# Performance work log

Hardware: AMD Instinct MI355X
Metric: run time of the kernel (lower is better)

The kernel has to match this reference:

```python
import jax, jax.numpy as jnp
import numpy as np

GROUP_MANTISSA = 8
GROUP_SIZE = 36


def bfp_quantize(x, mantissa=GROUP_MANTISSA, group_size=GROUP_SIZE):
    """Block floating point: flatten, group consecutive group_size elements,
    share the max exponent within each group, keep `mantissa` mantissa bits."""
    flat = x.reshape(-1)
    n = flat.shape[0]
    pad = (-n) % group_size
    f = jnp.pad(flat, (0, pad)).reshape(-1, group_size)  # [G, group_size]
    m = jnp.max(jnp.abs(f), axis=1, keepdims=True)       # group max magnitude
    safe_m = jnp.where(m > 0, m, jnp.ones_like(m))
    e = jnp.floor(jnp.log2(safe_m))                      # shared exponent
    scale = jnp.exp2(e - (mantissa - 1))                 # LSB step for the group
    q = jnp.round(f / scale) * scale
    q = jnp.where(m > 0, q, jnp.zeros_like(q))
    return q.reshape(-1)[:n].reshape(x.shape)


def setup_inputs() -> dict:
    key = jax.random.key(0)
    kx, kw, kb = jax.random.split(key, 3)
    x = jax.random.normal(kx, (32, 64, 112, 112), dtype=jnp.float32)
    # kaiming-uniform-ish scale for a 3x3x64 fan-in
    fan_in = 64 * 3 * 3
    bound = 1.0 / np.sqrt(fan_in)
    weight = jax.random.uniform(kw, (64, 64, 3, 3), dtype=jnp.float32, minval=-bound, maxval=bound) * np.sqrt(3.0)
    bias = jax.random.uniform(kb, (64,), dtype=jnp.float32, minval=-bound, maxval=bound)
    return {"x": x, "weight": weight, "bias": bias}


def reference(x, weight, bias):
    xq = bfp_quantize(x)
    wq = bfp_quantize(weight)
    out = jax.lax.conv_general_dilated(
        xq, wq,
        window_strides=(1, 1),
        padding=((1, 1), (1, 1)),
        lhs_dilation=(1, 1),
        rhs_dilation=(1, 1),
        dimension_numbers=("NCHW", "OIHW", "NCHW"),
        feature_group_count=1,
    )
    return out + bias[None, :, None, None]
```

## Files before the change

kernel.cpp:

```cpp
#include <hip/hip_runtime.h>
#include <hip/hip_bf16.h>

typedef __attribute__((ext_vector_type(4))) float f32x4;
typedef __attribute__((ext_vector_type(8))) short s16x8;

#define X_ELEMS 25690112
#define X_F4    6422528
#define NG_FULL 713614
#define NG      713615
#define HW 112
#define CHW (64*112*112)

__device__ __forceinline__ unsigned short f32_to_bf16_exact(float q) {
    return (unsigned short)(__float_as_uint(q) >> 16);
}

__device__ __forceinline__ void scale_from_max(float m, float& scale, float& inv) {
    if (m > 0.f) {
        int e = (int)((__float_as_uint(m) >> 23) & 0xFF) - 127;
        scale = __builtin_ldexpf(1.0f, e - 7);
        inv   = __builtin_ldexpf(1.0f, 7 - e);
    } else { scale = 0.f; inv = 0.f; }
}

__global__ __launch_bounds__(256) void q1_scales(const float* __restrict__ x,
                                                 float2* __restrict__ sc) {
    __shared__ float lmax[2304];
    int b = blockIdx.x, tid = threadIdx.x;
    long base4 = (long)b * 2304;
    #pragma unroll
    for (int it = 0; it < 9; ++it) {
        int i = it * 256 + tid;
        long g4 = base4 + i;
        float m = 0.f;
        if (g4 < X_F4) {
            float4 v = ((const float4*)x)[g4];
            m = fmaxf(fmaxf(fabsf(v.x), fabsf(v.y)), fmaxf(fabsf(v.z), fabsf(v.w)));
        }
        lmax[i] = m;
    }
    __syncthreads();
    int g = b * 256 + tid;
    if (g < NG) {
        float m = 0.f;
        int o = tid * 9;
        #pragma unroll
        for (int j = 0; j < 9; ++j) m = fmaxf(m, lmax[o + j]);
        float s, inv; scale_from_max(m, s, inv);
        sc[g] = make_float2(s, inv);
    }
}

__global__ __launch_bounds__(256) void qw_kernel(const float* __restrict__ w,
                                                 unsigned short* __restrict__ wt) {
    int g = blockIdx.x * 256 + threadIdx.x;
    if (g >= 1024) return;
    const float4* p = (const float4*)w + g * 9;
    float vv[36]; float m = 0.f;
    #pragma unroll
    for (int i = 0; i < 9; ++i) {
        float4 v = p[i];
        vv[i*4+0]=v.x; vv[i*4+1]=v.y; vv[i*4+2]=v.z; vv[i*4+3]=v.w;
        m = fmaxf(m, fmaxf(fmaxf(fabsf(v.x), fabsf(v.y)), fmaxf(fabsf(v.z), fabsf(v.w))));
    }
    float s, inv; scale_from_max(m, s, inv);
    #pragma unroll
    for (int j = 0; j < 36; ++j) {
        int flat = g * 36 + j;
        int k = flat / 576, rem = flat % 576;
        int c = rem / 9, pp = rem % 9;
        float q = rintf(vv[j] * inv) * s;
        wt[pp * 4096 + k * 64 + c] = f32_to_bf16_exact(q);
    }
}

__global__ __launch_bounds__(256) void q2_quant(const float* __restrict__ x,
                                               const float2* __restrict__ sc,
                                               unsigned short* __restrict__ xt) {
    int n = blockIdx.y, h = blockIdx.x;
    int tid = threadIdx.x;
    int cg = tid >> 7;
    int wv = tid & 127;
    if (wv >= HW) return;
    int base = n * CHW + h * HW + wv;
    int ob = ((n * HW + h) * HW + wv) * 64 + cg * 32;
    #pragma unroll
    for (int jo = 0; jo < 4; ++jo) {
        union { unsigned short u[8]; uint4 d; } pk;
        #pragma unroll
        for (int j = 0; j < 8; ++j) {
            int c = cg * 32 + jo * 8 + j;
            unsigned off = (unsigned)(base + c * 12544);
            float v = x[off];
            float2 s = sc[off / 36u];
            pk.u[j] = f32_to_bf16_exact(rintf(v * s.y) * s.x);
        }
        *(uint4*)(xt + ob + jo * 8) = pk.d;
    }
}

__global__ __launch_bounds__(256, 2) void conv_mfma(const unsigned short* __restrict__ xt,
                                                    const unsigned short* __restrict__ wt,
                                                    const float* __restrict__ bias,
                                                    float* __restrict__ out) {
    __shared__ unsigned short xs[300 * 72];
    const int tid = threadIdx.x;
    const int wave = tid >> 6, lane = tid & 63;
    const int wl = lane & 15, quad = lane >> 4;
    const int kg = wave & 1, mg = wave >> 1;
    const int b = blockIdx.x;
    const int n = b / 56, rem = b % 56;
    const int h0 = (rem >> 2) * 8, w0 = (rem & 3) * 28;

    #pragma unroll
    for (int it = 0; it < 10; ++it) {
        int q = it * 256 + tid;
        if (q < 2400) {
            int pixel = q >> 3, sub = q & 7;
            int r = pixel / 30, col = pixel % 30;
            int hh = h0 + r - 1, ww = w0 + col - 1;
            uint4 v = {0u, 0u, 0u, 0u};
            if (hh >= 0 && hh < HW && ww >= 0 && ww < HW)
                v = *(const uint4*)(xt + (((n * HW + hh) * HW + ww) << 6) + sub * 8);
            *(uint4*)&xs[pixel * 72 + sub * 8] = v;
        }
    }

    s16x8 Bf[9][2][2];
    #pragma unroll
    for (int p = 0; p < 9; ++p)
        #pragma unroll
        for (int cs = 0; cs < 2; ++cs)
            #pragma unroll
            for (int j = 0; j < 2; ++j)
                Bf[p][cs][j] = *(const s16x8*)(wt + p * 4096 +
                                ((kg * 2 + j) * 16 + wl) * 64 + cs * 32 + quad * 8);

    float bv[2];
    #pragma unroll
    for (int j = 0; j < 2; ++j) bv[j] = bias[kg * 32 + j * 16 + wl];

    int pixb[7], eofs[7];
    #pragma unroll
    for (int mti = 0; mti < 7; ++mti) {
        int m = (mg * 7 + mti) * 16 + wl;
        pixb[mti] = (m / 28) * 30 + (m % 28);
        int m0 = (mg * 7 + mti) * 16 + quad * 4;
        eofs[mti] = (m0 / 28) * HW + (m0 % 28);
    }

    __syncthreads();

    f32x4 acc[7][2];
    f32x4 zero = {0.f, 0.f, 0.f, 0.f};
    #pragma unroll
    for (int mti = 0; mti < 7; ++mti) { acc[mti][0] = zero; acc[mti][1] = zero; }

    #pragma unroll
    for (int p = 0; p < 9; ++p) {
        const int dpix = (p / 3) * 30 + (p % 3);
        #pragma unroll
        for (int cs = 0; cs < 2; ++cs) {
            const int cofs = cs * 32 + quad * 8;
            #pragma unroll
            for (int mti = 0; mti < 7; ++mti) {
                s16x8 A = *(const s16x8*)&xs[(pixb[mti] + dpix) * 72 + cofs];
                acc[mti][0] = __builtin_amdgcn_mfma_f32_16x16x32_bf16(A, Bf[p][cs][0], acc[mti][0], 0, 0, 0);
                acc[mti][1] = __builtin_amdgcn_mfma_f32_16x16x32_bf16(A, Bf[p][cs][1], acc[mti][1], 0, 0, 0);
            }
        }
    }

    int obase = n * CHW + h0 * HW + w0;
    #pragma unroll
    for (int mti = 0; mti < 7; ++mti) {
        #pragma unroll
        for (int j = 0; j < 2; ++j) {
            f32x4 v = acc[mti][j];
            v.x += bv[j]; v.y += bv[j]; v.z += bv[j]; v.w += bv[j];
            *(f32x4*)(out + obase + (kg * 32 + j * 16 + wl) * 12544 + eofs[mti]) = v;
        }
    }
}

extern "C" void kernel_launch(void* const* d_in, const int* in_sizes, int n_in,
                              void* d_out, int out_size, void* d_ws, size_t ws_size,
                              hipStream_t stream) {
    const float* x    = (const float*)d_in[0];
    const float* w    = (const float*)d_in[1];
    const float* bias = (const float*)d_in[2];
    float* out = (float*)d_out;
    char* ws = (char*)d_ws;
    unsigned short* xt = (unsigned short*)ws;
    unsigned short* wt = (unsigned short*)(ws + 51380224);
    float2*         sc = (float2*)(ws + 51380224 + 73728);

    hipLaunchKernelGGL(q1_scales, dim3(2788),    dim3(256), 0, stream, x, sc);
    hipLaunchKernelGGL(qw_kernel, dim3(4),       dim3(256), 0, stream, w, wt);
    hipLaunchKernelGGL(q2_quant,  dim3(112, 32), dim3(256), 0, stream, x, sc, xt);
    hipLaunchKernelGGL(conv_mfma, dim3(1792),    dim3(256), 0, stream, xt, wt, bias, out);
}
```

Measured before the change: 302.5 us.

## Fuse BFP quantization into one pass and transpose NCHW bf16 in conv staging

Merges the scale computation, weight quantization and activation quantization into a single kernel that keeps x in registers and writes quantized bf16 in the original NCHW layout. This drops the float2 scale buffer, the strided gather of the old quant kernel and two launches. The conv kernel now loads NCHW bf16 and transposes it into channel-last shared memory with byte permutes, using an XOR swizzle to reduce LDS bank conflicts. The cost is a more complex staging loop, a larger shared tile, and 8-byte strided global loads in the conv.

```diff
diff --git a/kernel.cpp b/kernel.cpp
--- a/kernel.cpp
+++ b/kernel.cpp
@@ -1,18 +1,21 @@
 #include <hip/hip_runtime.h>
-#include <hip/hip_bf16.h>
 
 typedef __attribute__((ext_vector_type(4))) float f32x4;
 typedef __attribute__((ext_vector_type(8))) short s16x8;
+typedef __attribute__((ext_vector_type(2))) unsigned int u32x2;
+typedef __attribute__((ext_vector_type(4))) unsigned int u32x4;
 
 #define X_ELEMS 25690112
 #define X_F4    6422528
-#define NG_FULL 713614
-#define NG      713615
 #define HW 112
 #define CHW (64*112*112)
 
 __device__ __forceinline__ unsigned short f32_to_bf16_exact(float q) {
     return (unsigned short)(__float_as_uint(q) >> 16);
+}
+
+__device__ __forceinline__ unsigned int pack_bf16x2(float a, float b) {
+    return __builtin_amdgcn_perm(__float_as_uint(b), __float_as_uint(a), 0x07060302u);
 }
 
 __device__ __forceinline__ void scale_from_max(float m, float& scale, float& inv) {
@@ -23,87 +26,85 @@
     } else { scale = 0.f; inv = 0.f; }
 }
 
-__global__ __launch_bounds__(256) void q1_scales(const float* __restrict__ x,
-                                                 float2* __restrict__ sc) {
+__global__ __launch_bounds__(256) void q1_quant(const float* __restrict__ x,
+                                                const float* __restrict__ w,
+                                                unsigned short* __restrict__ xq,
+                                                unsigned short* __restrict__ wt) {
     __shared__ float lmax[2304];
-    int b = blockIdx.x, tid = threadIdx.x;
+    __shared__ float lsc[256];
+    __shared__ float linv[256];
+    const int b = blockIdx.x, tid = threadIdx.x;
+
+    if (b == 2788) {
+        #pragma unroll 1
+        for (int rep = 0; rep < 4; ++rep) {
+            int g = rep * 256 + tid;
+            const float4* p = (const float4*)w + g * 9;
+            float vv[36]; float m = 0.f;
+            #pragma unroll
+            for (int i = 0; i < 9; ++i) {
+                float4 v = p[i];
+                vv[i*4+0]=v.x; vv[i*4+1]=v.y; vv[i*4+2]=v.z; vv[i*4+3]=v.w;
+                m = fmaxf(m, fmaxf(fmaxf(fabsf(v.x), fabsf(v.y)), fmaxf(fabsf(v.z), fabsf(v.w))));
+            }
+            float s, inv; scale_from_max(m, s, inv);
+            #pragma unroll
+            for (int j = 0; j < 36; ++j) {
+                int flat = g * 36 + j;
+                int k = flat / 576, rem = flat % 576;
+                int c = rem / 9, pp = rem % 9;
+                float q = rintf(vv[j] * inv) * s;
+                wt[pp * 4096 + k * 64 + c] = f32_to_bf16_exact(q);
+            }
+        }
+        return;
+    }
+
     long base4 = (long)b * 2304;
+    float4 vv[9];
     #pragma unroll
     for (int it = 0; it < 9; ++it) {
         int i = it * 256 + tid;
         long g4 = base4 + i;
-        float m = 0.f;
-        if (g4 < X_F4) {
-            float4 v = ((const float4*)x)[g4];
-            m = fmaxf(fmaxf(fabsf(v.x), fabsf(v.y)), fmaxf(fabsf(v.z), fabsf(v.w)));
-        }
-        lmax[i] = m;
+        float4 v = {0.f, 0.f, 0.f, 0.f};
+        if (g4 < X_F4) v = ((const float4*)x)[g4];
+        vv[it] = v;
+        lmax[i] = fmaxf(fmaxf(fabsf(v.x), fabsf(v.y)), fmaxf(fabsf(v.z), fabsf(v.w)));
     }
     __syncthreads();
-    int g = b * 256 + tid;
-    if (g < NG) {
-        float m = 0.f;
-        int o = tid * 9;
+    {
+        float m = 0.f; int o = tid * 9;
         #pragma unroll
         for (int j = 0; j < 9; ++j) m = fmaxf(m, lmax[o + j]);
         float s, inv; scale_from_max(m, s, inv);
-        sc[g] = make_float2(s, inv);
-    }
-}
-
-__global__ __launch_bounds__(256) void qw_kernel(const float* __restrict__ w,
-                                                 unsigned short* __restrict__ wt) {
-    int g = blockIdx.x * 256 + threadIdx.x;
-    if (g >= 1024) return;
-    const float4* p = (const float4*)w + g * 9;
-    float vv[36]; float m = 0.f;
-    #pragma unroll
-    for (int i = 0; i < 9; ++i) {
-        float4 v = p[i];
-        vv[i*4+0]=v.x; vv[i*4+1]=v.y; vv[i*4+2]=v.z; vv[i*4+3]=v.w;
-        m = fmaxf(m, fmaxf(fmaxf(fabsf(v.x), fabsf(v.y)), fmaxf(fabsf(v.z), fabsf(v.w))));
-    }
-    float s, inv; scale_from_max(m, s, inv);
-    #pragma unroll
-    for (int j = 0; j < 36; ++j) {
-        int flat = g * 36 + j;
-        int k = flat / 576, rem = flat % 576;
-        int c = rem / 9, pp = rem % 9;
-        float q = rintf(vv[j] * inv) * s;
-        wt[pp * 4096 + k * 64 + c] = f32_to_bf16_exact(q);
-    }
-}
-
-__global__ __launch_bounds__(256) void q2_quant(const float* __restrict__ x,
-                                               const float2* __restrict__ sc,
-                                               unsigned short* __restrict__ xt) {
-    int n = blockIdx.y, h = blockIdx.x;
-    int tid = threadIdx.x;
-    int cg = tid >> 7;
-    int wv = tid & 127;
-    if (wv >= HW) return;
-    int base = n * CHW + h * HW + wv;
-    int ob = ((n * HW + h) * HW + wv) * 64 + cg * 32;
-    #pragma unroll
-    for (int jo = 0; jo < 4; ++jo) {
-        union { unsigned short u[8]; uint4 d; } pk;
-        #pragma unroll
-        for (int j = 0; j < 8; ++j) {
-            int c = cg * 32 + jo * 8 + j;
-            unsigned off = (unsigned)(base + c * 12544);
-            float v = x[off];
-            float2 s = sc[off / 36u];
-            pk.u[j] = f32_to_bf16_exact(rintf(v * s.y) * s.x);
-        }
-        *(uint4*)(xt + ob + jo * 8) = pk.d;
-    }
-}
-
-__global__ __launch_bounds__(256, 2) void conv_mfma(const unsigned short* __restrict__ xt,
+        lsc[tid] = s; linv[tid] = inv;
+    }
+    __syncthreads();
+    #pragma unroll
+    for (int it = 0; it < 9; ++it) {
+        int i = it * 256 + tid;
+        long g4 = base4 + i;
+        if (g4 < X_F4) {
+            int lg = i / 9;
+            float s = lsc[lg], inv = linv[lg];
+            float4 v = vv[it];
+            u32x2 o;
+            o.x = pack_bf16x2(rintf(v.x * inv) * s, rintf(v.y * inv) * s);
+            o.y = pack_bf16x2(rintf(v.z * inv) * s, rintf(v.w * inv) * s);
+            *(u32x2*)(xq + g4 * 4) = o;
+        }
+    }
+}
+
+__device__ __forceinline__ int swz(int pix, int oct) {
+    return pix * 72 + (((oct) ^ ((pix >> 3) & 7)) << 3);
+}
+
+__global__ __launch_bounds__(256, 2) void conv_mfma(const unsigned short* __restrict__ xq,
                                                     const unsigned short* __restrict__ wt,
                                                     const float* __restrict__ bias,
                                                     float* __restrict__ out) {
-    __shared__ unsigned short xs[300 * 72];
+    __shared__ unsigned short xs[360 * 72];
     const int tid = threadIdx.x;
     const int wave = tid >> 6, lane = tid & 63;
     const int wl = lane & 15, quad = lane >> 4;
@@ -113,16 +114,35 @@
     const int h0 = (rem >> 2) * 8, w0 = (rem & 3) * 28;
 
     #pragma unroll
-    for (int it = 0; it < 10; ++it) {
-        int q = it * 256 + tid;
-        if (q < 2400) {
-            int pixel = q >> 3, sub = q & 7;
-            int r = pixel / 30, col = pixel % 30;
-            int hh = h0 + r - 1, ww = w0 + col - 1;
-            uint4 v = {0u, 0u, 0u, 0u};
-            if (hh >= 0 && hh < HW && ww >= 0 && ww < HW)
-                v = *(const uint4*)(xt + (((n * HW + hh) * HW + ww) << 6) + sub * 8);
-            *(uint4*)&xs[pixel * 72 + sub * 8] = v;
+    for (int tt = 0; tt < 3; ++tt) {
+        int t = tt * 256 + tid;
+        if (t < 720) {
+            int oct = t / 90;
+            int rm = t - oct * 90;
+            int r = rm / 9, i = rm - r * 9;
+            int hh = h0 - 1 + r;
+            int wb = w0 - 4 + i * 4;
+            u32x2 v[8];
+            if (hh >= 0 && hh < HW && wb >= 0 && wb <= 108) {
+                const unsigned short* src = xq + ((n * 64 + oct * 8) * HW + hh) * HW + wb;
+                #pragma unroll
+                for (int j = 0; j < 8; ++j)
+                    v[j] = *(const u32x2*)(src + j * 12544);
+            } else {
+                #pragma unroll
+                for (int j = 0; j < 8; ++j) v[j] = (u32x2){0u, 0u};
+            }
+            int pix0 = r * 36 + i * 4;
+            #pragma unroll
+            for (int d = 0; d < 4; ++d) {
+                unsigned int sel = (d & 1) ? 0x07060302u : 0x05040100u;
+                u32x4 o;
+                o.x = __builtin_amdgcn_perm(v[1][d >> 1], v[0][d >> 1], sel);
+                o.y = __builtin_amdgcn_perm(v[3][d >> 1], v[2][d >> 1], sel);
+                o.z = __builtin_amdgcn_perm(v[5][d >> 1], v[4][d >> 1], sel);
+                o.w = __builtin_amdgcn_perm(v[7][d >> 1], v[6][d >> 1], sel);
+                *(u32x4*)&xs[swz(pix0 + d, oct)] = o;
+            }
         }
     }
 
@@ -144,7 +164,7 @@
     #pragma unroll
     for (int mti = 0; mti < 7; ++mti) {
         int m = (mg * 7 + mti) * 16 + wl;
-        pixb[mti] = (m / 28) * 30 + (m % 28);
+        pixb[mti] = (m / 28) * 36 + (m % 28) + 3;
         int m0 = (mg * 7 + mti) * 16 + quad * 4;
         eofs[mti] = (m0 / 28) * HW + (m0 % 28);
     }
@@ -158,13 +178,13 @@
 
     #pragma unroll
     for (int p = 0; p < 9; ++p) {
-        const int dpix = (p / 3) * 30 + (p % 3);
-        #pragma unroll
-        for (int cs = 0; cs < 2; ++cs) {
-            const int cofs = cs * 32 + quad * 8;
-            #pragma unroll
-            for (int mti = 0; mti < 7; ++mti) {
-                s16x8 A = *(const s16x8*)&xs[(pixb[mti] + dpix) * 72 + cofs];
+        const int dpix = (p / 3) * 36 + (p % 3);
+        #pragma unroll
+        for (int mti = 0; mti < 7; ++mti) {
+            int pix = pixb[mti] + dpix;
+            #pragma unroll
+            for (int cs = 0; cs < 2; ++cs) {
+                s16x8 A = *(const s16x8*)&xs[swz(pix, cs * 4 + quad)];
                 acc[mti][0] = __builtin_amdgcn_mfma_f32_16x16x32_bf16(A, Bf[p][cs][0], acc[mti][0], 0, 0, 0);
                 acc[mti][1] = __builtin_amdgcn_mfma_f32_16x16x32_bf16(A, Bf[p][cs][1], acc[mti][1], 0, 0, 0);
             }
@@ -191,12 +211,9 @@
     const float* bias = (const float*)d_in[2];
     float* out = (float*)d_out;
     char* ws = (char*)d_ws;
-    unsigned short* xt = (unsigned short*)ws;
+    unsigned short* xq = (unsigned short*)ws;
     unsigned short* wt = (unsigned short*)(ws + 51380224);
-    float2*         sc = (float2*)(ws + 51380224 + 73728);
-
-    hipLaunchKernelGGL(q1_scales, dim3(2788),    dim3(256), 0, stream, x, sc);
-    hipLaunchKernelGGL(qw_kernel, dim3(4),       dim3(256), 0, stream, w, wt);
-    hipLaunchKernelGGL(q2_quant,  dim3(112, 32), dim3(256), 0, stream, x, sc, xt);
-    hipLaunchKernelGGL(conv_mfma, dim3(1792),    dim3(256), 0, stream, xt, wt, bias, out);
-}
+
+    hipLaunchKernelGGL(q1_quant,  dim3(2789), dim3(256), 0, stream, x, w, xq, wt);
+    hipLaunchKernelGGL(conv_mfma, dim3(1792), dim3(256), 0, stream, xq, wt, bias, out);
+}
```

Result: faster. 277.5 us (-8.2%).
